# Optimization experiments

Measured on AMD Instinct MI355X. Metric: run time of the kernel, lower is better.

## Reference

```python
import math
import jax, jax.numpy as jnp
import numpy as np

D_MODEL = 1024
NUM_HEADS = 16
HEAD_DIM = D_MODEL // NUM_HEADS
CAUSAL = True


def setup_inputs() -> dict:
    key = jax.random.key(0)
    ks = jax.random.split(key, 9)
    B, S = 2, 2048
    s = 1.0 / math.sqrt(D_MODEL)
    x = jax.random.normal(ks[0], (B, S, D_MODEL), dtype=jnp.float32)
    Wq = jax.random.normal(ks[1], (D_MODEL, D_MODEL), dtype=jnp.float32) * s
    bq = jax.random.normal(ks[2], (D_MODEL,), dtype=jnp.float32) * 0.01
    Wk = jax.random.normal(ks[3], (D_MODEL, D_MODEL), dtype=jnp.float32) * s
    bk = jax.random.normal(ks[4], (D_MODEL,), dtype=jnp.float32) * 0.01
    Wv = jax.random.normal(ks[5], (D_MODEL, D_MODEL), dtype=jnp.float32) * s
    bv = jax.random.normal(ks[6], (D_MODEL,), dtype=jnp.float32) * 0.01
    Wo = jax.random.normal(ks[7], (D_MODEL, D_MODEL), dtype=jnp.float32) * s
    bo = jax.random.normal(ks[8], (D_MODEL,), dtype=jnp.float32) * 0.01
    return {"x": x, "Wq": Wq, "bq": bq, "Wk": Wk, "bk": bk,
            "Wv": Wv, "bv": bv, "Wo": Wo, "bo": bo}


def reference(x, Wq, bq, Wk, bk, Wv, bv, Wo, bo):
    B, S, _ = x.shape
    # projections (torch Linear: x @ W.T + b; here W already stored as [in,out])
    q = x @ Wq + bq
    k = x @ Wk + bk
    v = x @ Wv + bv
    # split heads -> [B, H, S, hd]
    def split(t):
        return t.reshape(B, S, NUM_HEADS, HEAD_DIM).transpose(0, 2, 1, 3)
    q, k, v = split(q), split(k), split(v)
    scores = jnp.einsum('bhqd,bhkd->bhqk', q, k) / math.sqrt(HEAD_DIM)
    if CAUSAL:
        causal = jnp.tril(jnp.ones((S, S), dtype=bool))  # True = keep
        scores = jnp.where(causal, scores, -jnp.inf)
    attn = jax.nn.softmax(scores, axis=-1)
    out = jnp.einsum('bhqk,bhkd->bhqd', attn, v)
    out = out.transpose(0, 2, 1, 3).reshape(B, S, D_MODEL)
    return out @ Wo + bo
```

## Files before the change

### kernel.cpp

```cpp
#include <hip/hip_runtime.h>
#include <hip/hip_bf16.h>

typedef __bf16 bf16_t;
typedef __bf16 v8bf __attribute__((ext_vector_type(8)));
typedef float  v4f  __attribute__((ext_vector_type(4)));

#define MFMA16(a, b, c) __builtin_amdgcn_mfma_f32_16x16x32_bf16((a), (b), (c), 0, 0, 0)

#define GLDS16(g, l) __builtin_amdgcn_global_load_lds(                         \
    (const __attribute__((address_space(1))) void*)(g),                        \
    (__attribute__((address_space(3))) void*)(l), 16, 0, 0)

#define B_SZ   2
#define SEQ    2048
#define DM     1024
#define NH     16
#define HD     64
#define M_TOT  4096

#define QSCALE 0.18033688011112043f

__global__ __launch_bounds__(256)
void conv_x_kernel(const float* __restrict__ src, bf16_t* __restrict__ dst)
{
    int i = (blockIdx.x * 256 + threadIdx.x) * 8;
    float4 a = *reinterpret_cast<const float4*>(src + i);
    float4 b = *reinterpret_cast<const float4*>(src + i + 4);
    union { bf16_t h[8]; int4 v; } u;
    u.h[0] = (bf16_t)a.x; u.h[1] = (bf16_t)a.y; u.h[2] = (bf16_t)a.z; u.h[3] = (bf16_t)a.w;
    u.h[4] = (bf16_t)b.x; u.h[5] = (bf16_t)b.y; u.h[6] = (bf16_t)b.z; u.h[7] = (bf16_t)b.w;
    *reinterpret_cast<int4*>(dst + i) = u.v;
}

__global__ __launch_bounds__(256)
void conv_wt_kernel(const float* __restrict__ Wq, const float* __restrict__ Wk,
                    const float* __restrict__ Wv, const float* __restrict__ Wo,
                    bf16_t* __restrict__ WqkvT, bf16_t* __restrict__ WoT)
{
    __shared__ float t[32][33];
    const int z = blockIdx.z;
    const float* src = (z == 0) ? Wq : (z == 1) ? Wk : (z == 2) ? Wv : Wo;
    bf16_t* dst = (z < 3) ? (WqkvT + (size_t)z * 1048576) : WoT;
    const int tx = threadIdx.x & 31, ty = threadIdx.x >> 5;
    const int c0 = blockIdx.x * 32, r0 = blockIdx.y * 32;
#pragma unroll
    for (int i = 0; i < 4; ++i)
        t[ty + i * 8][tx] = src[(size_t)(r0 + ty + i * 8) * DM + c0 + tx];
    __syncthreads();
#pragma unroll
    for (int i = 0; i < 4; ++i)
        dst[(size_t)(c0 + ty + i * 8) * DM + r0 + tx] = (bf16_t)t[tx][ty + i * 8];
}

template <int MODE>
__global__ __launch_bounds__(256)
void gemm_bt_kernel(const bf16_t* __restrict__ A, const bf16_t* __restrict__ BT,
                    const float* __restrict__ b0, const float* __restrict__ b1,
                    const float* __restrict__ b2,
                    void* __restrict__ oQ, void* __restrict__ oK, void* __restrict__ oV)
{
    __shared__ __align__(16) bf16_t As[128 * 64];
    __shared__ __align__(16) bf16_t Bs[128 * 64];

    const int tid  = threadIdx.x;
    const int lane = tid & 63;
    const int wave = tid >> 6;
    const int wm   = (wave >> 1) * 64;
    const int wn   = (wave & 1) * 64;
    const int quad = lane >> 4;
    const int l15  = lane & 15;
    const int l7   = l15 & 7;

    int mat, n0;
    const bf16_t* Bmat;
    if (MODE == 1) { mat = blockIdx.x >> 3; n0 = (blockIdx.x & 7) * 128;
                     Bmat = BT + (size_t)mat * 1048576; }
    else           { mat = 0; n0 = blockIdx.x * 128; Bmat = BT; }
    const int m0 = blockIdx.y * 128;
    const bool transC = (MODE == 1) && (mat == 2);

    const v4f vzero = {0.f, 0.f, 0.f, 0.f};
    v4f acc[4][4];
#pragma unroll
    for (int mt = 0; mt < 4; ++mt)
#pragma unroll
        for (int nt = 0; nt < 4; ++nt) acc[mt][nt] = vzero;

    for (int it = 0; it < 16; ++it) {
        const int k0 = it * 64;
#pragma unroll
        for (int i = 0; i < 4; ++i) {
            int cidx = (wave * 4 + i) * 64 + lane;
            int r = cidx >> 3;
            int c = (cidx & 7) ^ (r & 7);
            GLDS16(A    + (size_t)(m0 + r) * DM + k0 + c * 8, As + (wave * 4 + i) * 512);
            GLDS16(Bmat + (size_t)(n0 + r) * DM + k0 + c * 8, Bs + (wave * 4 + i) * 512);
        }
        __syncthreads();
#pragma unroll
        for (int ks = 0; ks < 2; ++ks) {
            v8bf af[4], bfq[4];
#pragma unroll
            for (int mt = 0; mt < 4; ++mt)
                af[mt] = *reinterpret_cast<const v8bf*>(
                    &As[(wm + mt * 16 + l15) * 64 + ((ks * 4 + quad) ^ l7) * 8]);
#pragma unroll
            for (int nt = 0; nt < 4; ++nt)
                bfq[nt] = *reinterpret_cast<const v8bf*>(
                    &Bs[(wn + nt * 16 + l15) * 64 + ((ks * 4 + quad) ^ l7) * 8]);
            if (!transC) {
#pragma unroll
                for (int mt = 0; mt < 4; ++mt)
#pragma unroll
                    for (int nt = 0; nt < 4; ++nt)
                        acc[mt][nt] = MFMA16(af[mt], bfq[nt], acc[mt][nt]);
            } else {
#pragma unroll
                for (int mt = 0; mt < 4; ++mt)
#pragma unroll
                    for (int nt = 0; nt < 4; ++nt)
                        acc[mt][nt] = MFMA16(bfq[nt], af[mt], acc[mt][nt]);
            }
        }
        __syncthreads();
    }

    const float* bias = (MODE == 1) ? (mat == 0 ? b0 : mat == 1 ? b1 : b2) : b0;
    if (!transC) {
        const float scale = (MODE == 1 && mat == 0) ? QSCALE : 1.0f;
#pragma unroll
        for (int mt = 0; mt < 4; ++mt) {
#pragma unroll
            for (int nt = 0; nt < 4; ++nt) {
                int col = n0 + wn + nt * 16 + l15;
                float bv = bias[col];
#pragma unroll
                for (int r = 0; r < 4; ++r) {
                    int row = m0 + wm + mt * 16 + quad * 4 + r;
                    float v = (acc[mt][nt][r] + bv) * scale;
                    if (MODE == 0) {
                        reinterpret_cast<float*>(oQ)[(size_t)row * DM + col] = v;
                    } else {
                        int b = row >> 11, s = row & 2047;
                        int h = col >> 6,  d = col & 63;
                        bf16_t* dst = (mat == 0) ? (bf16_t*)oQ : (bf16_t*)oK;
                        dst[((size_t)(b * NH + h) * SEQ + s) * HD + d] = (bf16_t)v;
                    }
                }
            }
        }
    } else {
#pragma unroll
        for (int nt = 0; nt < 4; ++nt) {
#pragma unroll
            for (int r = 0; r < 4; ++r) {
                int coln = n0 + wn + nt * 16 + quad * 4 + r;
                float bv = bias[coln];
                int h = coln >> 6, d = coln & 63;
#pragma unroll
                for (int mt = 0; mt < 4; ++mt) {
                    int srow = m0 + wm + mt * 16 + l15;
                    int b = srow >> 11, s = srow & 2047;
                    reinterpret_cast<bf16_t*>(oV)[
                        ((size_t)(b * NH + h) * HD + d) * SEQ + s] =
                        (bf16_t)(acc[mt][nt][r] + bv);
                }
            }
        }
    }
}

__global__ __launch_bounds__(256)
void attn_kernel(const bf16_t* __restrict__ Q, const bf16_t* __restrict__ K,
                 const bf16_t* __restrict__ Vt, bf16_t* __restrict__ O)
{
    __shared__ __align__(16) bf16_t Ks[64 * 64];
    __shared__ __align__(16) bf16_t Vs[64 * 64];
    __shared__ __align__(16) bf16_t Ps[64 * 72];

    const int tid  = threadIdx.x;
    const int lane = tid & 63;
    const int w    = tid >> 6;
    const int quad = lane >> 4;
    const int l15  = lane & 15;
    const int l7   = lane & 7;

    const int x = blockIdx.x, y = blockIdx.y;
    const int u_ = (x + (y & 24)) & 31;
    const int r_ = u_ >> 3, s_ = u_ & 7;
    const int t  = (r_ == 0) ? s_ : (r_ == 1) ? 31 - s_ : (r_ == 2) ? 8 + s_ : 23 - s_;
    const int bh = y;
    const int q0 = t * 64;
    const size_t base = (size_t)bh * SEQ * HD;

    const bf16_t* Qg = Q  + base;
    const bf16_t* Kg = K  + base;
    const bf16_t* Vg = Vt + base;

    v8bf qf[2];
    {
        const bf16_t* qrow = Qg + (size_t)(q0 + w * 16 + l15) * HD;
        qf[0] = *reinterpret_cast<const v8bf*>(qrow + quad * 8);
        qf[1] = *reinterpret_cast<const v8bf*>(qrow + 32 + quad * 8);
    }

    const v4f vzero = {0.f, 0.f, 0.f, 0.f};
    v4f acc_o[4];
#pragma unroll
    for (int dt = 0; dt < 4; ++dt) acc_o[dt] = vzero;
    float mrow = -1e30f, lrow = 0.f;
    const int qg = q0 + w * 16 + l15;

    for (int kt = 0; kt <= t; ++kt) {
        {
            const bf16_t* Kt0 = Kg + (size_t)kt * 64 * HD;
            const bf16_t* Vt0 = Vg + kt * 64;
#pragma unroll
            for (int i = 0; i < 2; ++i) {
                int cidx = i * 256 + tid;
                int rr = cidx >> 3;
                int cc = (cidx & 7) ^ (rr & 7);
                GLDS16(Kt0 + (size_t)rr * HD  + cc * 8, Ks + (i * 256 + w * 64) * 8);
                GLDS16(Vt0 + (size_t)rr * SEQ + cc * 8, Vs + (i * 256 + w * 64) * 8);
            }
        }
        __syncthreads();

        v4f st[4];
#pragma unroll
        for (int ktile = 0; ktile < 4; ++ktile) st[ktile] = vzero;
#pragma unroll
        for (int ks = 0; ks < 2; ++ks) {
            v8bf kb[4];
#pragma unroll
            for (int ktile = 0; ktile < 4; ++ktile)
                kb[ktile] = *reinterpret_cast<const v8bf*>(
                    &Ks[(ktile * 16 + l15) * 64 + ((ks * 4 + quad) ^ l7) * 8]);
#pragma unroll
            for (int ktile = 0; ktile < 4; ++ktile)
                st[ktile] = MFMA16(kb[ktile], qf[ks], st[ktile]);
        }

        const bool diagI = (kt == t);
        float rm = -1e30f;
#pragma unroll
        for (int ktile = 0; ktile < 4; ++ktile) {
            if (diagI && ktile > w) continue;
#pragma unroll
            for (int r = 0; r < 4; ++r) {
                float v = st[ktile][r];
                if (diagI && ktile == w) {
                    int kg = kt * 64 + ktile * 16 + quad * 4 + r;
                    if (kg > qg) v = -1e30f;
                }
                st[ktile][r] = v;
                rm = fmaxf(rm, v);
            }
        }
        rm = fmaxf(rm, __shfl_xor(rm, 16));
        rm = fmaxf(rm, __shfl_xor(rm, 32));
        float mn = fmaxf(mrow, rm);
        float alpha = exp2f(mrow - mn);
        mrow = mn;
        float rs = 0.f;
        const int prow = (w * 16 + l15) * 72;
#pragma unroll
        for (int ktile = 0; ktile < 4; ++ktile) {
            union { bf16_t h[4]; int2 v; } u;
            if (diagI && ktile > w) {
                u.v.x = 0; u.v.y = 0;
            } else {
#pragma unroll
                for (int r = 0; r < 4; ++r) {
                    float p = exp2f(st[ktile][r] - mn);
                    rs += p;
                    u.h[r] = (bf16_t)p;
                }
            }
            *reinterpret_cast<int2*>(&Ps[prow + ktile * 16 + quad * 4]) = u.v;
        }
        rs += __shfl_xor(rs, 16);
        rs += __shfl_xor(rs, 32);
        lrow = lrow * alpha + rs;
#pragma unroll
        for (int dt = 0; dt < 4; ++dt)
#pragma unroll
            for (int r = 0; r < 4; ++r)
                acc_o[dt][r] *= alpha;

#pragma unroll
        for (int ks = 0; ks < 2; ++ks) {
            v8bf vb[4];
#pragma unroll
            for (int dt = 0; dt < 4; ++dt)
                vb[dt] = *reinterpret_cast<const v8bf*>(
                    &Vs[(dt * 16 + l15) * 64 + ((ks * 4 + quad) ^ l7) * 8]);
            v8bf pf = *reinterpret_cast<const v8bf*>(
                &Ps[(w * 16 + l15) * 72 + ks * 32 + quad * 8]);
#pragma unroll
            for (int dt = 0; dt < 4; ++dt)
                acc_o[dt] = MFMA16(vb[dt], pf, acc_o[dt]);
        }
        __syncthreads();
    }

    const int bO = bh >> 4, hO = bh & 15;
    float rinv = 1.f / lrow;
    int s = q0 + w * 16 + l15;
#pragma unroll
    for (int dt = 0; dt < 4; ++dt) {
        union { bf16_t h[4]; int2 v; } u;
#pragma unroll
        for (int r = 0; r < 4; ++r)
            u.h[r] = (bf16_t)(acc_o[dt][r] * rinv);
        *reinterpret_cast<int2*>(
            &O[((size_t)bO * SEQ + s) * DM + hO * 64 + dt * 16 + quad * 4]) = u.v;
    }
}

extern "C" void kernel_launch(void* const* d_in, const int* in_sizes, int n_in,
                              void* d_out, int out_size, void* d_ws, size_t ws_size,
                              hipStream_t stream) {
    const float* x  = (const float*)d_in[0];
    const float* Wq = (const float*)d_in[1];
    const float* bq = (const float*)d_in[2];
    const float* Wk = (const float*)d_in[3];
    const float* bk = (const float*)d_in[4];
    const float* Wv = (const float*)d_in[5];
    const float* bv = (const float*)d_in[6];
    const float* Wo = (const float*)d_in[7];
    const float* bo = (const float*)d_in[8];

    bf16_t* ws = (bf16_t*)d_ws;
    bf16_t* xb     = ws;
    bf16_t* WqkvT  = ws + 4194304;
    bf16_t* WoT    = ws + 7340032;
    bf16_t* Qb     = ws + 8388608;
    bf16_t* Kb     = ws + 12582912;
    bf16_t* Vb     = ws + 16777216;
    bf16_t* Ob     = ws;

    conv_x_kernel<<<2048, 256, 0, stream>>>(x, xb);
    conv_wt_kernel<<<dim3(32, 32, 4), 256, 0, stream>>>(Wq, Wk, Wv, Wo, WqkvT, WoT);
    gemm_bt_kernel<1><<<dim3(24, 32), 256, 0, stream>>>(xb, WqkvT, bq, bk, bv, Qb, Kb, Vb);
    attn_kernel<<<dim3(32, 32), 256, 0, stream>>>(Qb, Kb, Vb, Ob);
    gemm_bt_kernel<0><<<dim3(8, 32), 256, 0, stream>>>(Ob, WoT, bo, nullptr, nullptr,
                                                       d_out, nullptr, nullptr);
}
```

Before: 215.0 us.

## Split causal attention KV range in two with a separate combine kernel

Each query tile's causal KV range is split into two halves handled by separate blocks, launched longest-first. Each block writes unnormalized bf16 partial outputs plus per-row max and sum. A new combine kernel merges the two halves with log-sum-exp weights and writes the normalized output. This is meant to give more parallelism and better load balance than the earlier tile-permutation scheme. The cost is an extra launch, extra global traffic for the partials, and rounding the partials to bf16. The GEMM and attention loads also now use pointers computed once and incremented, instead of recomputing addresses every iteration.

```diff
diff --git a/kernel.cpp b/kernel.cpp
--- a/kernel.cpp
+++ b/kernel.cpp
@@ -79,6 +79,16 @@
     const int m0 = blockIdx.y * 128;
     const bool transC = (MODE == 1) && (mat == 2);
 
+    const bf16_t *ap[4], *bp[4];
+#pragma unroll
+    for (int i = 0; i < 4; ++i) {
+        int cidx = (wave * 4 + i) * 64 + lane;
+        int r = cidx >> 3;
+        int c = (cidx & 7) ^ (r & 7);
+        ap[i] = A    + (size_t)(m0 + r) * DM + c * 8;
+        bp[i] = Bmat + (size_t)(n0 + r) * DM + c * 8;
+    }
+
     const v4f vzero = {0.f, 0.f, 0.f, 0.f};
     v4f acc[4][4];
 #pragma unroll
@@ -87,14 +97,11 @@
         for (int nt = 0; nt < 4; ++nt) acc[mt][nt] = vzero;
 
     for (int it = 0; it < 16; ++it) {
-        const int k0 = it * 64;
 #pragma unroll
         for (int i = 0; i < 4; ++i) {
-            int cidx = (wave * 4 + i) * 64 + lane;
-            int r = cidx >> 3;
-            int c = (cidx & 7) ^ (r & 7);
-            GLDS16(A    + (size_t)(m0 + r) * DM + k0 + c * 8, As + (wave * 4 + i) * 512);
-            GLDS16(Bmat + (size_t)(n0 + r) * DM + k0 + c * 8, Bs + (wave * 4 + i) * 512);
+            GLDS16(ap[i], As + (wave * 4 + i) * 512);
+            GLDS16(bp[i], Bs + (wave * 4 + i) * 512);
+            ap[i] += 64; bp[i] += 64;
         }
         __syncthreads();
 #pragma unroll
@@ -172,7 +179,8 @@
 
 __global__ __launch_bounds__(256)
 void attn_kernel(const bf16_t* __restrict__ Q, const bf16_t* __restrict__ K,
-                 const bf16_t* __restrict__ Vt, bf16_t* __restrict__ O)
+                 const bf16_t* __restrict__ Vt, bf16_t* __restrict__ Opart,
+                 float* __restrict__ ml)
 {
     __shared__ __align__(16) bf16_t Ks[64 * 64];
     __shared__ __align__(16) bf16_t Vs[64 * 64];
@@ -185,12 +193,16 @@
     const int l15  = lane & 15;
     const int l7   = lane & 7;
 
-    const int x = blockIdx.x, y = blockIdx.y;
-    const int u_ = (x + (y & 24)) & 31;
-    const int r_ = u_ >> 3, s_ = u_ & 7;
-    const int t  = (r_ == 0) ? s_ : (r_ == 1) ? 31 - s_ : (r_ == 2) ? 8 + s_ : 23 - s_;
-    const int bh = y;
-    const int q0 = t * 64;
+    const int x    = blockIdx.x;
+    const int bh   = blockIdx.y;
+    const int t    = 31 - (x >> 1);
+    const int half = x & 1;
+    const int n    = t + 1;
+    const int h0   = (n + 1) >> 1;
+    const int lo   = half ? h0 : 0;
+    const int hi   = half ? n  : h0;
+    const int pidx = (bh * 32 + t) * 2 + half;
+    const int q0   = t * 64;
     const size_t base = (size_t)bh * SEQ * HD;
 
     const bf16_t* Qg = Q  + base;
@@ -204,6 +216,15 @@
         qf[1] = *reinterpret_cast<const v8bf*>(qrow + 32 + quad * 8);
     }
 
+    const int rr0 = tid >> 3;
+    const int cc0 = (tid & 7) ^ (rr0 & 7);
+    const bf16_t* kp0 = Kg + (size_t)lo * 64 * HD + (size_t)rr0 * HD + cc0 * 8;
+    const bf16_t* kp1 = kp0 + 32 * HD;
+    const bf16_t* vp0 = Vg + (size_t)rr0 * SEQ + (size_t)lo * 64 + cc0 * 8;
+    const bf16_t* vp1 = vp0 + (size_t)32 * SEQ;
+    bf16_t* dK0 = Ks + w * 512;          bf16_t* dK1 = Ks + 2048 + w * 512;
+    bf16_t* dV0 = Vs + w * 512;          bf16_t* dV1 = Vs + 2048 + w * 512;
+
     const v4f vzero = {0.f, 0.f, 0.f, 0.f};
     v4f acc_o[4];
 #pragma unroll
@@ -211,19 +232,10 @@
     float mrow = -1e30f, lrow = 0.f;
     const int qg = q0 + w * 16 + l15;
 
-    for (int kt = 0; kt <= t; ++kt) {
-        {
-            const bf16_t* Kt0 = Kg + (size_t)kt * 64 * HD;
-            const bf16_t* Vt0 = Vg + kt * 64;
-#pragma unroll
-            for (int i = 0; i < 2; ++i) {
-                int cidx = i * 256 + tid;
-                int rr = cidx >> 3;
-                int cc = (cidx & 7) ^ (rr & 7);
-                GLDS16(Kt0 + (size_t)rr * HD  + cc * 8, Ks + (i * 256 + w * 64) * 8);
-                GLDS16(Vt0 + (size_t)rr * SEQ + cc * 8, Vs + (i * 256 + w * 64) * 8);
-            }
-        }
+    for (int kt = lo; kt < hi; ++kt) {
+        GLDS16(kp0, dK0);  GLDS16(kp1, dK1);
+        GLDS16(vp0, dV0);  GLDS16(vp1, dV1);
+        kp0 += 64 * HD;  kp1 += 64 * HD;  vp0 += 64;  vp1 += 64;
         __syncthreads();
 
         v4f st[4];
@@ -304,17 +316,48 @@
         __syncthreads();
     }
 
-    const int bO = bh >> 4, hO = bh & 15;
-    float rinv = 1.f / lrow;
-    int s = q0 + w * 16 + l15;
+    const int q = w * 16 + l15;
+    bf16_t* ob = Opart + ((size_t)pidx * 64 + q) * 64;
 #pragma unroll
     for (int dt = 0; dt < 4; ++dt) {
         union { bf16_t h[4]; int2 v; } u;
 #pragma unroll
         for (int r = 0; r < 4; ++r)
-            u.h[r] = (bf16_t)(acc_o[dt][r] * rinv);
-        *reinterpret_cast<int2*>(
-            &O[((size_t)bO * SEQ + s) * DM + hO * 64 + dt * 16 + quad * 4]) = u.v;
+            u.h[r] = (bf16_t)acc_o[dt][r];
+        *reinterpret_cast<int2*>(ob + dt * 16 + quad * 4) = u.v;
+    }
+    if (quad == 0) {
+        ml[pidx * 128 + q]      = mrow;
+        ml[pidx * 128 + 64 + q] = lrow;
+    }
+}
+
+__global__ __launch_bounds__(256)
+void attn_combine(const bf16_t* __restrict__ Opart, const float* __restrict__ ml,
+                  bf16_t* __restrict__ O)
+{
+    const int t = blockIdx.x, bh = blockIdx.y;
+    const int tid = threadIdx.x;
+    const int q = tid >> 2, dg = (tid & 3) * 16;
+    const int p0 = (bh * 32 + t) * 2;
+    const float m1 = ml[p0 * 128 + q],       l1 = ml[p0 * 128 + 64 + q];
+    const float m2 = ml[p0 * 128 + 128 + q], l2 = ml[p0 * 128 + 192 + q];
+    const float M  = fmaxf(m1, m2);
+    const float w1 = exp2f(m1 - M), w2 = exp2f(m2 - M);
+    const float rinv = 1.f / (w1 * l1 + w2 * l2);
+    const size_t b1 = ((size_t)p0 * 64 + q) * 64 + dg;
+    const size_t b2 = b1 + 4096;
+    const int bO = bh >> 4, hO = bh & 15;
+    bf16_t* dst = O + ((size_t)bO * SEQ + t * 64 + q) * DM + hO * 64 + dg;
+#pragma unroll
+    for (int h = 0; h < 2; ++h) {
+        v8bf a = *reinterpret_cast<const v8bf*>(Opart + b1 + h * 8);
+        v8bf b = *reinterpret_cast<const v8bf*>(Opart + b2 + h * 8);
+        union { bf16_t hh[8]; int4 v; } u;
+#pragma unroll
+        for (int r = 0; r < 8; ++r)
+            u.hh[r] = (bf16_t)(((float)a[r] * w1 + (float)b[r] * w2) * rinv);
+        *reinterpret_cast<int4*>(dst + h * 8) = u.v;
     }
 }
 
@@ -334,16 +377,19 @@
     bf16_t* ws = (bf16_t*)d_ws;
     bf16_t* xb     = ws;
     bf16_t* WqkvT  = ws + 4194304;
-    bf16_t* WoT    = ws + 7340032;
-    bf16_t* Qb     = ws + 8388608;
-    bf16_t* Kb     = ws + 12582912;
-    bf16_t* Vb     = ws + 16777216;
-    bf16_t* Ob     = ws;
+    bf16_t* Opart  = ws;
+    float*  mlbuf  = (float*)(ws + 8388608);
+    bf16_t* WoT    = ws + 8912896;
+    bf16_t* Qb     = ws + 9961472;
+    bf16_t* Kb     = ws + 14155776;
+    bf16_t* Vb     = ws + 18350080;
+    bf16_t* Ob     = Qb;
 
     conv_x_kernel<<<2048, 256, 0, stream>>>(x, xb);
     conv_wt_kernel<<<dim3(32, 32, 4), 256, 0, stream>>>(Wq, Wk, Wv, Wo, WqkvT, WoT);
     gemm_bt_kernel<1><<<dim3(24, 32), 256, 0, stream>>>(xb, WqkvT, bq, bk, bv, Qb, Kb, Vb);
-    attn_kernel<<<dim3(32, 32), 256, 0, stream>>>(Qb, Kb, Vb, Ob);
+    attn_kernel<<<dim3(64, 32), 256, 0, stream>>>(Qb, Kb, Vb, Opart, mlbuf);
+    attn_combine<<<dim3(32, 32), 256, 0, stream>>>(Opart, mlbuf, Ob);
     gemm_bt_kernel<0><<<dim3(8, 32), 256, 0, stream>>>(Ob, WoT, bo, nullptr, nullptr,
                                                        d_out, nullptr, nullptr);
 }
```

Result: slower. 231.9 us (+7.9%).

## Split GEMM kernels, vectorize QKV stores, hoist load addresses, shrink output-GEMM tiles

Applied to the files above, without the earlier changes.

The templated GEMM becomes two kernels. The QKV kernel always uses the transposed MFMA operand order, so Q and K can be written with packed 8-byte bf16 stores and a float4 bias load instead of scalar stores. The output projection moves to a 128x64 tile, doubling the grid from 256 to 512 blocks so more of the CUs have work, at the cost of more A re-reads. The attention and GEMM K-loops compute global load pointers once and increment them, replacing per-iteration address arithmetic.

```diff
diff --git a/kernel.cpp b/kernel.cpp
--- a/kernel.cpp
+++ b/kernel.cpp
@@ -52,12 +52,12 @@
         dst[(size_t)(c0 + ty + i * 8) * DM + r0 + tx] = (bf16_t)t[tx][ty + i * 8];
 }
 
-template <int MODE>
 __global__ __launch_bounds__(256)
-void gemm_bt_kernel(const bf16_t* __restrict__ A, const bf16_t* __restrict__ BT,
-                    const float* __restrict__ b0, const float* __restrict__ b1,
-                    const float* __restrict__ b2,
-                    void* __restrict__ oQ, void* __restrict__ oK, void* __restrict__ oV)
+void gemm_qkv_kernel(const bf16_t* __restrict__ A, const bf16_t* __restrict__ BT,
+                     const float* __restrict__ b0, const float* __restrict__ b1,
+                     const float* __restrict__ b2,
+                     bf16_t* __restrict__ oQ, bf16_t* __restrict__ oK,
+                     bf16_t* __restrict__ oV)
 {
     __shared__ __align__(16) bf16_t As[128 * 64];
     __shared__ __align__(16) bf16_t Bs[128 * 64];
@@ -71,13 +71,20 @@
     const int l15  = lane & 15;
     const int l7   = l15 & 7;
 
-    int mat, n0;
-    const bf16_t* Bmat;
-    if (MODE == 1) { mat = blockIdx.x >> 3; n0 = (blockIdx.x & 7) * 128;
-                     Bmat = BT + (size_t)mat * 1048576; }
-    else           { mat = 0; n0 = blockIdx.x * 128; Bmat = BT; }
-    const int m0 = blockIdx.y * 128;
-    const bool transC = (MODE == 1) && (mat == 2);
+    const int mat = blockIdx.x >> 3;
+    const int n0  = (blockIdx.x & 7) * 128;
+    const int m0  = blockIdx.y * 128;
+    const bf16_t* Bmat = BT + (size_t)mat * 1048576;
+
+    const bf16_t *ap[4], *bp[4];
+#pragma unroll
+    for (int i = 0; i < 4; ++i) {
+        int cidx = (wave * 4 + i) * 64 + lane;
+        int r = cidx >> 3;
+        int c = (cidx & 7) ^ (r & 7);
+        ap[i] = A    + (size_t)(m0 + r) * DM + c * 8;
+        bp[i] = Bmat + (size_t)(n0 + r) * DM + c * 8;
+    }
 
     const v4f vzero = {0.f, 0.f, 0.f, 0.f};
     v4f acc[4][4];
@@ -87,14 +94,11 @@
         for (int nt = 0; nt < 4; ++nt) acc[mt][nt] = vzero;
 
     for (int it = 0; it < 16; ++it) {
-        const int k0 = it * 64;
 #pragma unroll
         for (int i = 0; i < 4; ++i) {
-            int cidx = (wave * 4 + i) * 64 + lane;
-            int r = cidx >> 3;
-            int c = (cidx & 7) ^ (r & 7);
-            GLDS16(A    + (size_t)(m0 + r) * DM + k0 + c * 8, As + (wave * 4 + i) * 512);
-            GLDS16(Bmat + (size_t)(n0 + r) * DM + k0 + c * 8, Bs + (wave * 4 + i) * 512);
+            GLDS16(ap[i], As + (wave * 4 + i) * 512);
+            GLDS16(bp[i], Bs + (wave * 4 + i) * 512);
+            ap[i] += 64; bp[i] += 64;
         }
         __syncthreads();
 #pragma unroll
@@ -108,45 +112,35 @@
             for (int nt = 0; nt < 4; ++nt)
                 bfq[nt] = *reinterpret_cast<const v8bf*>(
                     &Bs[(wn + nt * 16 + l15) * 64 + ((ks * 4 + quad) ^ l7) * 8]);
-            if (!transC) {
-#pragma unroll
-                for (int mt = 0; mt < 4; ++mt)
-#pragma unroll
-                    for (int nt = 0; nt < 4; ++nt)
-                        acc[mt][nt] = MFMA16(af[mt], bfq[nt], acc[mt][nt]);
-            } else {
-#pragma unroll
-                for (int mt = 0; mt < 4; ++mt)
-#pragma unroll
-                    for (int nt = 0; nt < 4; ++nt)
-                        acc[mt][nt] = MFMA16(bfq[nt], af[mt], acc[mt][nt]);
-            }
-        }
-        __syncthreads();
-    }
-
-    const float* bias = (MODE == 1) ? (mat == 0 ? b0 : mat == 1 ? b1 : b2) : b0;
-    if (!transC) {
-        const float scale = (MODE == 1 && mat == 0) ? QSCALE : 1.0f;
-#pragma unroll
-        for (int mt = 0; mt < 4; ++mt) {
-#pragma unroll
-            for (int nt = 0; nt < 4; ++nt) {
-                int col = n0 + wn + nt * 16 + l15;
-                float bv = bias[col];
-#pragma unroll
-                for (int r = 0; r < 4; ++r) {
-                    int row = m0 + wm + mt * 16 + quad * 4 + r;
-                    float v = (acc[mt][nt][r] + bv) * scale;
-                    if (MODE == 0) {
-                        reinterpret_cast<float*>(oQ)[(size_t)row * DM + col] = v;
-                    } else {
-                        int b = row >> 11, s = row & 2047;
-                        int h = col >> 6,  d = col & 63;
-                        bf16_t* dst = (mat == 0) ? (bf16_t*)oQ : (bf16_t*)oK;
-                        dst[((size_t)(b * NH + h) * SEQ + s) * HD + d] = (bf16_t)v;
-                    }
-                }
+#pragma unroll
+            for (int mt = 0; mt < 4; ++mt)
+#pragma unroll
+                for (int nt = 0; nt < 4; ++nt)
+                    acc[mt][nt] = MFMA16(bfq[nt], af[mt], acc[mt][nt]);
+        }
+        __syncthreads();
+    }
+
+    const float* bias = (mat == 0) ? b0 : (mat == 1) ? b1 : b2;
+    if (mat != 2) {
+        bf16_t* dst = (mat == 0) ? oQ : oK;
+        const float scale = (mat == 0) ? QSCALE : 1.0f;
+        const int h = (n0 + wn) >> 6;
+#pragma unroll
+        for (int nt = 0; nt < 4; ++nt) {
+            const int dbase = nt * 16 + quad * 4;
+            float4 bv = *reinterpret_cast<const float4*>(bias + n0 + wn + dbase);
+#pragma unroll
+            for (int mt = 0; mt < 4; ++mt) {
+                int srow = m0 + wm + mt * 16 + l15;
+                int b = srow >> 11, s = srow & 2047;
+                union { bf16_t hh[4]; int2 v; } u;
+                u.hh[0] = (bf16_t)((acc[mt][nt][0] + bv.x) * scale);
+                u.hh[1] = (bf16_t)((acc[mt][nt][1] + bv.y) * scale);
+                u.hh[2] = (bf16_t)((acc[mt][nt][2] + bv.z) * scale);
+                u.hh[3] = (bf16_t)((acc[mt][nt][3] + bv.w) * scale);
+                *reinterpret_cast<int2*>(
+                    dst + ((size_t)(b * NH + h) * SEQ + s) * HD + dbase) = u.v;
             }
         }
     } else {
@@ -161,10 +155,98 @@
                 for (int mt = 0; mt < 4; ++mt) {
                     int srow = m0 + wm + mt * 16 + l15;
                     int b = srow >> 11, s = srow & 2047;
-                    reinterpret_cast<bf16_t*>(oV)[
-                        ((size_t)(b * NH + h) * HD + d) * SEQ + s] =
+                    oV[((size_t)(b * NH + h) * HD + d) * SEQ + s] =
                         (bf16_t)(acc[mt][nt][r] + bv);
                 }
+            }
+        }
+    }
+}
+
+__global__ __launch_bounds__(256)
+void gemm_o_kernel(const bf16_t* __restrict__ A, const bf16_t* __restrict__ BT,
+                   const float* __restrict__ bias, float* __restrict__ out)
+{
+    __shared__ __align__(16) bf16_t As[128 * 64];
+    __shared__ __align__(16) bf16_t Bs[64 * 64];
+
+    const int tid  = threadIdx.x;
+    const int lane = tid & 63;
+    const int wave = tid >> 6;
+    const int wm   = (wave >> 1) * 64;
+    const int wn   = (wave & 1) * 32;
+    const int quad = lane >> 4;
+    const int l15  = lane & 15;
+    const int l7   = l15 & 7;
+
+    const int n0 = blockIdx.x * 64;
+    const int m0 = blockIdx.y * 128;
+
+    const bf16_t *ap[4], *bp[2];
+#pragma unroll
+    for (int i = 0; i < 4; ++i) {
+        int cidx = (wave * 4 + i) * 64 + lane;
+        int r = cidx >> 3;
+        int c = (cidx & 7) ^ (r & 7);
+        ap[i] = A + (size_t)(m0 + r) * DM + c * 8;
+    }
+#pragma unroll
+    for (int i = 0; i < 2; ++i) {
+        int cidx = (wave * 2 + i) * 64 + lane;
+        int r = cidx >> 3;
+        int c = (cidx & 7) ^ (r & 7);
+        bp[i] = BT + (size_t)(n0 + r) * DM + c * 8;
+    }
+
+    const v4f vzero = {0.f, 0.f, 0.f, 0.f};
+    v4f acc[4][2];
+#pragma unroll
+    for (int mt = 0; mt < 4; ++mt)
+#pragma unroll
+        for (int nt = 0; nt < 2; ++nt) acc[mt][nt] = vzero;
+
+    for (int it = 0; it < 16; ++it) {
+#pragma unroll
+        for (int i = 0; i < 4; ++i) {
+            GLDS16(ap[i], As + (wave * 4 + i) * 512);
+            ap[i] += 64;
+        }
+#pragma unroll
+        for (int i = 0; i < 2; ++i) {
+            GLDS16(bp[i], Bs + (wave * 2 + i) * 512);
+            bp[i] += 64;
+        }
+        __syncthreads();
+#pragma unroll
+        for (int ks = 0; ks < 2; ++ks) {
+            v8bf af[4], bfq[2];
+#pragma unroll
+            for (int mt = 0; mt < 4; ++mt)
+                af[mt] = *reinterpret_cast<const v8bf*>(
+                    &As[(wm + mt * 16 + l15) * 64 + ((ks * 4 + quad) ^ l7) * 8]);
+#pragma unroll
+            for (int nt = 0; nt < 2; ++nt)
+                bfq[nt] = *reinterpret_cast<const v8bf*>(
+                    &Bs[(wn + nt * 16 + l15) * 64 + ((ks * 4 + quad) ^ l7) * 8]);
+#pragma unroll
+            for (int mt = 0; mt < 4; ++mt)
+#pragma unroll
+                for (int nt = 0; nt < 2; ++nt)
+                    acc[mt][nt] = MFMA16(af[mt], bfq[nt], acc[mt][nt]);
+        }
+        __syncthreads();
+    }
+
+#pragma unroll
+    for (int mt = 0; mt < 4; ++mt) {
+#pragma unroll
+        for (int nt = 0; nt < 2; ++nt) {
+            int col = n0 + wn + nt * 16 + l15;
+            float bv = bias[col];
+#pragma unroll
+            for (int r = 0; r < 4; ++r) {
+                int row = m0 + wm + mt * 16 + quad * 4 + r;
+                out[(size_t)row * DM + col] = acc[mt][nt][r] + bv;
             }
         }
     }
@@ -204,6 +286,15 @@
         qf[1] = *reinterpret_cast<const v8bf*>(qrow + 32 + quad * 8);
     }
 
+    const int rr0 = tid >> 3;
+    const int cc0 = (tid & 7) ^ (rr0 & 7);
+    const bf16_t* kp0 = Kg + (size_t)rr0 * HD + cc0 * 8;
+    const bf16_t* kp1 = kp0 + 32 * HD;
+    const bf16_t* vp0 = Vg + (size_t)rr0 * SEQ + cc0 * 8;
+    const bf16_t* vp1 = vp0 + (size_t)32 * SEQ;
+    bf16_t* dK0 = Ks + w * 512;          bf16_t* dK1 = Ks + 2048 + w * 512;
+    bf16_t* dV0 = Vs + w * 512;          bf16_t* dV1 = Vs + 2048 + w * 512;
+
     const v4f vzero = {0.f, 0.f, 0.f, 0.f};
     v4f acc_o[4];
 #pragma unroll
@@ -212,18 +303,9 @@
     const int qg = q0 + w * 16 + l15;
 
     for (int kt = 0; kt <= t; ++kt) {
-        {
-            const bf16_t* Kt0 = Kg + (size_t)kt * 64 * HD;
-            const bf16_t* Vt0 = Vg + kt * 64;
-#pragma unroll
-            for (int i = 0; i < 2; ++i) {
-                int cidx = i * 256 + tid;
-                int rr = cidx >> 3;
-                int cc = (cidx & 7) ^ (rr & 7);
-                GLDS16(Kt0 + (size_t)rr * HD  + cc * 8, Ks + (i * 256 + w * 64) * 8);
-                GLDS16(Vt0 + (size_t)rr * SEQ + cc * 8, Vs + (i * 256 + w * 64) * 8);
-            }
-        }
+        GLDS16(kp0, dK0);  GLDS16(kp1, dK1);
+        GLDS16(vp0, dV0);  GLDS16(vp1, dV1);
+        kp0 += 64 * HD;  kp1 += 64 * HD;  vp0 += 64;  vp1 += 64;
         __syncthreads();
 
         v4f st[4];
@@ -342,8 +424,7 @@
 
     conv_x_kernel<<<2048, 256, 0, stream>>>(x, xb);
     conv_wt_kernel<<<dim3(32, 32, 4), 256, 0, stream>>>(Wq, Wk, Wv, Wo, WqkvT, WoT);
-    gemm_bt_kernel<1><<<dim3(24, 32), 256, 0, stream>>>(xb, WqkvT, bq, bk, bv, Qb, Kb, Vb);
+    gemm_qkv_kernel<<<dim3(24, 32), 256, 0, stream>>>(xb, WqkvT, bq, bk, bv, Qb, Kb, Vb);
     attn_kernel<<<dim3(32, 32), 256, 0, stream>>>(Qb, Kb, Vb, Ob);
-    gemm_bt_kernel<0><<<dim3(8, 32), 256, 0, stream>>>(Ob, WoT, bo, nullptr, nullptr,
-                                                       d_out, nullptr, nullptr);
-}
+    gemm_o_kernel<<<dim3(16, 32), 256, 0, stream>>>(Ob, WoT, bo, (float*)d_out);
+}
```

Measured after the change: 225.9 us. +5.1%, slower.
